# Kernel tuning notes

Measured on AMD Instinct MI355X. Metric: run time of the kernel, lower is better.

## Reference

```python
import jax, jax.numpy as jnp
import numpy as np

# config constants
S = 26            # output_size (fm_width == fm_height)
A = 5             # anchor_num
C = 80            # class_num
B = 64            # batch_size
T = 16            # GT boxes per image
DS = 32.0         # downsample_rate
IOU_THR = 0.5
SCALE_NOOBJ = 1.0
SCALE_OBJ = 5.0
ANCHOR_BOX = np.array([[1.32, 1.73], [3.19, 4.0], [5.05, 8.09], [9.47, 4.84], [11.2, 10.0]], dtype=np.float32)


def setup_inputs() -> dict:
    key = jax.random.key(0)
    ks = jax.random.split(key, 8)
    conf = jax.random.normal(ks[0], (B, S, S, A, 1), dtype=jnp.float32)
    pred_xy = jax.random.uniform(ks[1], (B, S, S, A, 2), dtype=jnp.float32) * S
    pred_wh = jax.random.uniform(ks[2], (B, S, S, A, 2), dtype=jnp.float32) * S + 0.5
    cls_score = jax.random.normal(ks[3], (B, S, S, A, C), dtype=jnp.float32)
    # GT boxes in PIXEL coords (module divides by downsample_rate): (x, y, w, h)
    xy = jax.random.uniform(ks[4], (B, T, 2), dtype=jnp.float32) * (S * DS)
    wh = jax.random.uniform(ks[5], (B, T, 2), dtype=jnp.float32) * (S * DS * 0.5) + DS
    true_object = jnp.concatenate([xy, wh], axis=-1)
    cls_idx = jax.random.randint(ks[6], (B, T), 0, C)
    true_label = jax.nn.one_hot(cls_idx, C, dtype=jnp.float32)
    # per-cell integer coords, row-major over the S*S grid
    p = jnp.arange(S * S)
    fm_cord = jnp.stack([p // S, p % S], axis=-1).astype(jnp.float32)  # [S*S, 2]
    anchors = jnp.asarray(ANCHOR_BOX)
    epoch = 1
    return {"epoch": epoch, "conf": conf, "pred_xy": pred_xy, "pred_wh": pred_wh,
            "cls_score": cls_score, "true_object": true_object, "true_label": true_label,
            "fm_cord": fm_cord, "anchors": anchors}


def _center_align_iou_wh(wh1, wh2):
    # IoU of two boxes whose centers are aligned: only (w, h) matter.
    inter = jnp.minimum(wh1[..., 0], wh2[..., 0]) * jnp.minimum(wh1[..., 1], wh2[..., 1])
    union = wh1[..., 0] * wh1[..., 1] + wh2[..., 0] * wh2[..., 1] - inter
    return inter / union


def _bce_with_logits(x, t):
    return jnp.maximum(x, 0.0) - x * t + jnp.log1p(jnp.exp(-jnp.abs(x)))


def _assign_targets(pred_wh, true_object, true_label, anchors):
    """Vectorized replacement of the per-box Python loops."""
    g = true_object / DS                                   # [B,T,4] in fm units
    gw, gh = g[..., 2], g[..., 3]
    i = jnp.clip(jnp.floor(g[..., 0]).astype(jnp.int32), 0, S - 1)  # int(x)
    j = jnp.clip(jnp.floor(g[..., 1]).astype(jnp.int32), 0, S - 1)  # int(y)
    b_idx = jnp.broadcast_to(jnp.arange(B)[:, None], (B, T))

    # anchor-vs-gt center-aligned IoU: [B,T,A]
    inter = jnp.minimum(gw[..., None], anchors[:, 0]) * jnp.minimum(gh[..., None], anchors[:, 1])
    union = (gw * gh)[..., None] + anchors[:, 0] * anchors[:, 1] - inter
    iou_a = inter / union
    best = jnp.argmax(iou_a, axis=-1)                      # [B,T]

    # predicted box at the BEST anchor cell (the original uses best_iou_index in
    # both the if- and else- branches), center-aligned IoU against the gt box
    pbest_wh = pred_wh[b_idx, i, j, best]                  # [B,T,2]
    iou_pg = _center_align_iou_wh(pbest_wh, g[..., 2:4])   # [B,T]

    aa = jnp.broadcast_to(jnp.arange(A), (B, T, A))
    is_best = aa == best[..., None]
    over = iou_a > IOU_THR
    scale_best = 2.0 - (gw / S) * (gh / S)                 # [B,T]

    mask_val = jnp.where(is_best, 1.0, jnp.where(over, -1.0, 0.0))
    scale_val = jnp.where(is_best, scale_best[..., None], jnp.where(over, -1.0, 0.0))

    bi = jnp.broadcast_to(b_idx[..., None], (B, T, A))
    ii = jnp.broadcast_to(i[..., None], (B, T, A))
    jj = jnp.broadcast_to(j[..., None], (B, T, A))

    obj_mask = jnp.zeros((B, S, S, A), jnp.float32).at[bi, ii, jj, aa].set(mask_val)
    scale_weight = jnp.zeros((B, S, S, A), jnp.float32).at[bi, ii, jj, aa].set(scale_val)

    # pred_gt_iou is written for the best anchor and for non-best anchors BELOW
    # the threshold (else-branch); over-threshold non-best anchors are skipped.
    write_iou = is_best | (~over)
    a_safe = jnp.where(write_iou, aa, A)  # out-of-bounds -> dropped
    pred_gt_iou = jnp.zeros((B, S, S, A), jnp.float32).at[bi, ii, jj, a_safe].set(
        jnp.broadcast_to(iou_pg[..., None], (B, T, A)), mode="drop")

    true_bbox = jnp.zeros((B, S, S, A, 4), jnp.float32).at[b_idx, i, j, best].set(g)
    true_score = jnp.zeros((B, S, S, A, C), jnp.float32).at[..., -1].set(1.0)
    true_score = true_score.at[b_idx, i, j, best].set(true_label)
    return obj_mask, scale_weight, pred_gt_iou, true_bbox, true_score


def _yolo_loss(epoch, conf, pred_xy, pred_wh, cls_score, true_object, true_label, fm_cord, anchors):
    obj_mask, scale_weight, pred_gt_iou, true_bbox, true_score = _assign_targets(
        pred_wh, true_object, true_label, anchors)

    N = S * S * A
    conf_f = conf.reshape(B, N, 1)
    pxy = pred_xy.reshape(B, N, 2)
    pwh = pred_wh.reshape(B, N, 2)
    tb = true_bbox.reshape(B, N, 4)
    m = obj_mask.reshape(B, N, 1)
    piou = pred_gt_iou.reshape(B, N, 1)
    sw = scale_weight.reshape(B, N, 1)
    ts = true_score.reshape(B, N, C).transpose(0, 2, 1)    # [B,C,N]
    cs = cls_score.reshape(B, N, C).transpose(0, 2, 1)     # [B,C,N]
    # mimics fm_cord.view(WH,2).repeat(1,A,1): whole grid tiled A times -> [N,2]
    fm = jnp.tile(fm_cord, (A, 1))

    noobj_loss = (SCALE_NOOBJ * (m == 0) * 0.5 * conf_f ** 2).sum() / B
    obj_loss = (SCALE_OBJ * (m == 1) * 0.5 * (conf_f - piou) ** 2).sum() / B
    gt_mask = (sw > 0).astype(conf.dtype)
    true_loss_xy = (SCALE_OBJ * 0.5 * gt_mask * sw *
                    _bce_with_logits(pxy - fm[None], tb[..., :2] - fm[None])).sum() / B
    true_loss_wh = (SCALE_OBJ * 0.5 * gt_mask * sw * (pwh - tb[..., 2:]) ** 2).sum() / B
    cls_gt_mask = gt_mask.transpose(0, 2, 1)               # [B,1,N]
    score_loss = (SCALE_OBJ * 0.5 * cls_gt_mask * (cs - ts) ** 2).sum() / B
    # NOTE: original code computes the averaged total then OVERWRITES it:
    total_loss = score_loss
    return (total_loss, noobj_loss / 4.0, obj_loss / 4.0, score_loss / 4.0,
            true_loss_xy / 4.0, true_loss_wh / 4.0)


def reference(epoch, conf, pred_xy, pred_wh, cls_score, true_object, true_label, fm_cord, anchors):
    return _yolo_loss(epoch, conf, pred_xy, pred_wh, cls_score, true_object, true_label, fm_cord, anchors)
```

## Files before the change

### kernel.cpp

```cpp
#include <hip/hip_runtime.h>
#include <math.h>

#define S 26
#define A 5
#define C 80
#define B 64
#define T 16
#define DSR 32.0f
#define N_CELLS (S * S)
#define N_PRED (S * S * A)
#define CONF_N (B * N_PRED)
#define CONF_N4 (CONF_N / 4)
#define NBT (B * T)
#define NBLK 256
#define BS 256
#define NWAVE (BS / 64)

__global__ __launch_bounds__(BS) void main_kernel(
        const float* __restrict__ conf,
        const float* __restrict__ pred_xy,
        const float* __restrict__ pred_wh,
        const float* __restrict__ cls_score,
        const float* __restrict__ true_object,
        const float* __restrict__ true_label,
        const float* __restrict__ anchors,
        float* __restrict__ partials) {
    const int tid = threadIdx.x;
    const int bid = blockIdx.x;
    const int gidx = bid * BS + tid;
    const int lane = tid & 63;
    const int wave = tid >> 6;

    float v0 = 0.f, v1 = 0.f, v2 = 0.f, v3 = 0.f, v4 = 0.f, v5 = 0.f;

    if (gidx < CONF_N4) {
        float4 c = ((const float4*)conf)[gidx];
        v0 = c.x * c.x + c.y * c.y + c.z * c.z + c.w * c.w;
    }

    if (gidx < NBT) {
        const int bt = gidx;
        const int b = bt >> 4;
        const int t = bt & 15;

        float4 to = ((const float4*)true_object)[bt];
        float gx = to.x / DSR, gy = to.y / DSR;
        float gw = to.z / DSR, gh = to.w / DSR;
        int i = min(max((int)floorf(gx), 0), S - 1);
        int j = min(max((int)floorf(gy), 0), S - 1);
        int ij = i * S + j;

        bool winner = true;
        #pragma unroll
        for (int t2 = 0; t2 < T; ++t2) {
            int ij2 = __shfl(ij, (lane & 48) + t2, 64);
            if (t2 > t && ij2 == ij) winner = false;
        }

        if (winner) {
            float iou_a[A];
            int best = 0;
            float bestv = -1.f;
            #pragma unroll
            for (int a = 0; a < A; ++a) {
                float aw = anchors[a * 2 + 0], ah = anchors[a * 2 + 1];
                float inter = fminf(gw, aw) * fminf(gh, ah);
                float uni = gw * gh + aw * ah - inter;
                float val = inter / uni;
                iou_a[a] = val;
                if (val > bestv) { bestv = val; best = a; }
            }

            size_t base = (size_t)b * N_PRED + (size_t)ij * A;

            #pragma unroll
            for (int a = 0; a < A; ++a) {
                if (a == best || iou_a[a] > 0.5f) {
                    float c = conf[base + a];
                    v1 += 0.5f * c * c;
                }
            }

            float2 pwh = ((const float2*)pred_wh)[base + best];
            float pw = pwh.x, ph = pwh.y;
            float inter = fminf(pw, gw) * fminf(ph, gh);
            float uni = pw * ph + gw * gh - inter;
            float iou_pg = inter / uni;
            float cbest = conf[base + best];
            float d = cbest - iou_pg;
            v2 = 0.5f * d * d;

            float sw = 2.0f - (gw / (float)S) * (gh / (float)S);
            if (sw > 0.f) {
                int n = ij * A + best;
                int p = n % N_CELLS;
                float fm0 = (float)(p / S);
                float fm1 = (float)(p % S);
                float2 pxy = ((const float2*)pred_xy)[base + best];
                float x0 = pxy.x - fm0, tt0 = gx - fm0;
                float x1 = pxy.y - fm1, tt1 = gy - fm1;
                float bce0 = fmaxf(x0, 0.f) - x0 * tt0 + log1pf(expf(-fabsf(x0)));
                float bce1 = fmaxf(x1, 0.f) - x1 * tt1 + log1pf(expf(-fabsf(x1)));
                v3 = sw * (bce0 + bce1);
                float dw = pw - gw, dh = ph - gh;
                v4 = sw * (dw * dw + dh * dh);

                const float4* cs4 = (const float4*)(cls_score + (base + best) * C);
                const float4* tl4 = (const float4*)(true_label + (size_t)bt * C);
                float sacc = 0.f;
                #pragma unroll
                for (int c4 = 0; c4 < C / 4; ++c4) {
                    float4 cc = cs4[c4];
                    float4 tl = tl4[c4];
                    float d0 = cc.x - tl.x, d1 = cc.y - tl.y;
                    float d2 = cc.z - tl.z, d3 = cc.w - tl.w;
                    sacc += d0 * d0 + d1 * d1 + d2 * d2 + d3 * d3;
                }
                v5 = sacc;
            }
        }
    }

    float vs[6] = {v0, v1, v2, v3, v4, v5};
    #pragma unroll
    for (int k = 0; k < 6; ++k) {
        float v = vs[k];
        #pragma unroll
        for (int off = 32; off >= 1; off >>= 1)
            v += __shfl_xor(v, off, 64);
        vs[k] = v;
    }
    __shared__ float sm[NWAVE * 6];
    if (lane == 0) {
        #pragma unroll
        for (int k = 0; k < 6; ++k) sm[wave * 6 + k] = vs[k];
    }
    __syncthreads();
    if (tid < 6) {
        float s = 0.f;
        #pragma unroll
        for (int w = 0; w < NWAVE; ++w) s += sm[w * 6 + tid];
        partials[tid * NBLK + bid] = s;
    }
}

__global__ __launch_bounds__(64) void finalize_kernel(
        const float* __restrict__ partials, float* __restrict__ out) {
    const int tid = threadIdx.x;
    float sums[6];
    #pragma unroll
    for (int k = 0; k < 6; ++k) {
        const float* p = partials + k * NBLK;
        float v = p[tid] + p[tid + 64] + p[tid + 128] + p[tid + 192];
        #pragma unroll
        for (int off = 32; off >= 1; off >>= 1)
            v += __shfl_xor(v, off, 64);
        sums[k] = v;
    }
    if (tid == 0) {
        const float invB = 1.0f / (float)B;
        float noobj = (0.5f * sums[0] - sums[1]) * invB;
        float obj   = 5.0f * sums[2] * invB;
        float xy    = 2.5f * sums[3] * invB;
        float wh    = 2.5f * sums[4] * invB;
        float score = 2.5f * sums[5] * invB;
        out[0] = score;
        out[1] = noobj * 0.25f;
        out[2] = obj * 0.25f;
        out[3] = score * 0.25f;
        out[4] = xy * 0.25f;
        out[5] = wh * 0.25f;
    }
}

extern "C" void kernel_launch(void* const* d_in, const int* in_sizes, int n_in,
                              void* d_out, int out_size, void* d_ws, size_t ws_size,
                              hipStream_t stream) {
    const float* conf        = (const float*)d_in[1];
    const float* pred_xy     = (const float*)d_in[2];
    const float* pred_wh     = (const float*)d_in[3];
    const float* cls_score   = (const float*)d_in[4];
    const float* true_object = (const float*)d_in[5];
    const float* true_label  = (const float*)d_in[6];
    const float* anchors     = (const float*)d_in[8];

    float* ws  = (float*)d_ws;
    float* out = (float*)d_out;

    hipLaunchKernelGGL(main_kernel, dim3(NBLK), dim3(BS), 0, stream,
                       conf, pred_xy, pred_wh, cls_score, true_object,
                       true_label, anchors, ws);
    hipLaunchKernelGGL(finalize_kernel, dim3(1), dim3(64), 0, stream, ws, out);
}
```

Measured before the change: 13.22 us.

## Fuse finalize into main kernel via flag-tagged partials polled by block zero

Merges the two-kernel reduction into one launch. Block 0 spins on per-block 64-bit packets tagged with a magic value and reduces them, then resets the flags for the next call. Worker blocks now split their work by range, so the GT-box threads are a separate slice after the conf slice and 216 worker blocks are used instead of 256. This removes the second launch and its gap, but depends on all 217 blocks being co-resident to avoid deadlock, and on the workspace not holding stale magic values.

New measurement: 14.05 us. 1.06x slower.

```diff
diff --git a/kernel.cpp b/kernel.cpp
--- a/kernel.cpp
+++ b/kernel.cpp
@@ -12,11 +12,13 @@
 #define CONF_N (B * N_PRED)
 #define CONF_N4 (CONF_N / 4)
 #define NBT (B * T)
-#define NBLK 256
 #define BS 256
-#define NWAVE (BS / 64)
-
-__global__ __launch_bounds__(BS) void main_kernel(
+#define NWORK 216
+#define NBLK (NWORK + 1)
+#define NFLAGS (NWORK * 6)
+#define MAGIC 0x9E3779B9u
+
+__global__ __launch_bounds__(BS) void yolo_fused(
         const float* __restrict__ conf,
         const float* __restrict__ pred_xy,
         const float* __restrict__ pred_wh,
@@ -24,104 +26,150 @@
         const float* __restrict__ true_object,
         const float* __restrict__ true_label,
         const float* __restrict__ anchors,
-        float* __restrict__ partials) {
+        unsigned long long* __restrict__ flags,
+        float* __restrict__ out) {
     const int tid = threadIdx.x;
     const int bid = blockIdx.x;
-    const int gidx = bid * BS + tid;
     const int lane = tid & 63;
     const int wave = tid >> 6;
-
-    float v0 = 0.f, v1 = 0.f, v2 = 0.f, v3 = 0.f, v4 = 0.f, v5 = 0.f;
-
-    if (gidx < CONF_N4) {
-        float4 c = ((const float4*)conf)[gidx];
-        v0 = c.x * c.x + c.y * c.y + c.z * c.z + c.w * c.w;
-    }
-
-    if (gidx < NBT) {
-        const int bt = gidx;
-        const int b = bt >> 4;
-        const int t = bt & 15;
-
-        float4 to = ((const float4*)true_object)[bt];
-        float gx = to.x / DSR, gy = to.y / DSR;
-        float gw = to.z / DSR, gh = to.w / DSR;
-        int i = min(max((int)floorf(gx), 0), S - 1);
-        int j = min(max((int)floorf(gy), 0), S - 1);
-        int ij = i * S + j;
-
-        bool winner = true;
-        #pragma unroll
-        for (int t2 = 0; t2 < T; ++t2) {
-            int ij2 = __shfl(ij, (lane & 48) + t2, 64);
-            if (t2 > t && ij2 == ij) winner = false;
-        }
-
-        if (winner) {
-            float iou_a[A];
-            int best = 0;
-            float bestv = -1.f;
+    __shared__ float sm[(BS / 64) * 6];
+
+    if (bid > 0) {
+        const int gidx = (bid - 1) * BS + tid;
+        float v0 = 0.f, v1 = 0.f, v2 = 0.f, v3 = 0.f, v4 = 0.f, v5 = 0.f;
+
+        if (gidx < CONF_N4) {
+            float4 c = ((const float4*)conf)[gidx];
+            v0 = c.x * c.x + c.y * c.y + c.z * c.z + c.w * c.w;
+        } else if (gidx < CONF_N4 + NBT) {
+            const int bt = gidx - CONF_N4;
+            const int b = bt >> 4;
+            const int t = bt & 15;
+
+            float4 to = ((const float4*)true_object)[bt];
+            float gx = to.x / DSR, gy = to.y / DSR;
+            float gw = to.z / DSR, gh = to.w / DSR;
+            int i = min(max((int)floorf(gx), 0), S - 1);
+            int j = min(max((int)floorf(gy), 0), S - 1);
+            int ij = i * S + j;
+
+            bool winner = true;
             #pragma unroll
-            for (int a = 0; a < A; ++a) {
-                float aw = anchors[a * 2 + 0], ah = anchors[a * 2 + 1];
-                float inter = fminf(gw, aw) * fminf(gh, ah);
-                float uni = gw * gh + aw * ah - inter;
-                float val = inter / uni;
-                iou_a[a] = val;
-                if (val > bestv) { bestv = val; best = a; }
+            for (int t2 = 0; t2 < T; ++t2) {
+                int ij2 = __shfl(ij, (lane & 48) + t2, 64);
+                if (t2 > t && ij2 == ij) winner = false;
             }
 
-            size_t base = (size_t)b * N_PRED + (size_t)ij * A;
-
-            #pragma unroll
-            for (int a = 0; a < A; ++a) {
-                if (a == best || iou_a[a] > 0.5f) {
-                    float c = conf[base + a];
-                    v1 += 0.5f * c * c;
+            if (winner) {
+                float iou_a[A];
+                int best = 0;
+                float bestv = -1.f;
+                #pragma unroll
+                for (int a = 0; a < A; ++a) {
+                    float aw = anchors[a * 2 + 0], ah = anchors[a * 2 + 1];
+                    float inter = fminf(gw, aw) * fminf(gh, ah);
+                    float uni = gw * gh + aw * ah - inter;
+                    float val = inter / uni;
+                    iou_a[a] = val;
+                    if (val > bestv) { bestv = val; best = a; }
+                }
+
+                size_t base = (size_t)b * N_PRED + (size_t)ij * A;
+
+                #pragma unroll
+                for (int a = 0; a < A; ++a) {
+                    if (a == best || iou_a[a] > 0.5f) {
+                        float c = conf[base + a];
+                        v1 += 0.5f * c * c;
+                    }
+                }
+
+                float2 pwh = ((const float2*)pred_wh)[base + best];
+                float pw = pwh.x, ph = pwh.y;
+                float inter = fminf(pw, gw) * fminf(ph, gh);
+                float uni = pw * ph + gw * gh - inter;
+                float iou_pg = inter / uni;
+                float cbest = conf[base + best];
+                float d = cbest - iou_pg;
+                v2 = 0.5f * d * d;
+
+                float sw = 2.0f - (gw / (float)S) * (gh / (float)S);
+                if (sw > 0.f) {
+                    int n = ij * A + best;
+                    int p = n % N_CELLS;
+                    float fm0 = (float)(p / S);
+                    float fm1 = (float)(p % S);
+                    float2 pxy = ((const float2*)pred_xy)[base + best];
+                    float x0 = pxy.x - fm0, tt0 = gx - fm0;
+                    float x1 = pxy.y - fm1, tt1 = gy - fm1;
+                    float bce0 = fmaxf(x0, 0.f) - x0 * tt0 + log1pf(expf(-fabsf(x0)));
+                    float bce1 = fmaxf(x1, 0.f) - x1 * tt1 + log1pf(expf(-fabsf(x1)));
+                    v3 = sw * (bce0 + bce1);
+                    float dw = pw - gw, dh = ph - gh;
+                    v4 = sw * (dw * dw + dh * dh);
+
+                    const float4* cs4 = (const float4*)(cls_score + (base + best) * C);
+                    const float4* tl4 = (const float4*)(true_label + (size_t)bt * C);
+                    float sacc = 0.f;
+                    #pragma unroll
+                    for (int c4 = 0; c4 < C / 4; ++c4) {
+                        float4 cc = cs4[c4];
+                        float4 tl = tl4[c4];
+                        float d0 = cc.x - tl.x, d1 = cc.y - tl.y;
+                        float d2 = cc.z - tl.z, d3 = cc.w - tl.w;
+                        sacc += d0 * d0 + d1 * d1 + d2 * d2 + d3 * d3;
+                    }
+                    v5 = sacc;
                 }
             }
-
-            float2 pwh = ((const float2*)pred_wh)[base + best];
-            float pw = pwh.x, ph = pwh.y;
-            float inter = fminf(pw, gw) * fminf(ph, gh);
-            float uni = pw * ph + gw * gh - inter;
-            float iou_pg = inter / uni;
-            float cbest = conf[base + best];
-            float d = cbest - iou_pg;
-            v2 = 0.5f * d * d;
-
-            float sw = 2.0f - (gw / (float)S) * (gh / (float)S);
-            if (sw > 0.f) {
-                int n = ij * A + best;
-                int p = n % N_CELLS;
-                float fm0 = (float)(p / S);
-                float fm1 = (float)(p % S);
-                float2 pxy = ((const float2*)pred_xy)[base + best];
-                float x0 = pxy.x - fm0, tt0 = gx - fm0;
-                float x1 = pxy.y - fm1, tt1 = gy - fm1;
-                float bce0 = fmaxf(x0, 0.f) - x0 * tt0 + log1pf(expf(-fabsf(x0)));
-                float bce1 = fmaxf(x1, 0.f) - x1 * tt1 + log1pf(expf(-fabsf(x1)));
-                v3 = sw * (bce0 + bce1);
-                float dw = pw - gw, dh = ph - gh;
-                v4 = sw * (dw * dw + dh * dh);
-
-                const float4* cs4 = (const float4*)(cls_score + (base + best) * C);
-                const float4* tl4 = (const float4*)(true_label + (size_t)bt * C);
-                float sacc = 0.f;
-                #pragma unroll
-                for (int c4 = 0; c4 < C / 4; ++c4) {
-                    float4 cc = cs4[c4];
-                    float4 tl = tl4[c4];
-                    float d0 = cc.x - tl.x, d1 = cc.y - tl.y;
-                    float d2 = cc.z - tl.z, d3 = cc.w - tl.w;
-                    sacc += d0 * d0 + d1 * d1 + d2 * d2 + d3 * d3;
-                }
-                v5 = sacc;
-            }
-        }
-    }
-
-    float vs[6] = {v0, v1, v2, v3, v4, v5};
+        }
+
+        float vs[6] = {v0, v1, v2, v3, v4, v5};
+        #pragma unroll
+        for (int k = 0; k < 6; ++k) {
+            float v = vs[k];
+            #pragma unroll
+            for (int off = 32; off >= 1; off >>= 1)
+                v += __shfl_xor(v, off, 64);
+            vs[k] = v;
+        }
+        if (lane == 0) {
+            #pragma unroll
+            for (int k = 0; k < 6; ++k) sm[wave * 6 + k] = vs[k];
+        }
+        __syncthreads();
+        if (tid < 6) {
+            float s = sm[0 * 6 + tid] + sm[1 * 6 + tid] +
+                      sm[2 * 6 + tid] + sm[3 * 6 + tid];
+            unsigned long long pkt =
+                ((unsigned long long)MAGIC << 32) |
+                (unsigned long long)__float_as_uint(s);
+            __hip_atomic_store(&flags[(bid - 1) * 6 + tid], pkt,
+                               __ATOMIC_RELEASE, __HIP_MEMORY_SCOPE_AGENT);
+        }
+        return;
+    }
+
+    float s0 = 0.f, s1 = 0.f, s2 = 0.f, s3 = 0.f, s4 = 0.f, s5 = 0.f;
+    for (int m = tid; m < NFLAGS; m += BS) {
+        unsigned long long v;
+        do {
+            v = __hip_atomic_load(&flags[m], __ATOMIC_ACQUIRE,
+                                  __HIP_MEMORY_SCOPE_AGENT);
+        } while ((unsigned)(v >> 32) != MAGIC);
+        __hip_atomic_store(&flags[m], 0ull, __ATOMIC_RELAXED,
+                           __HIP_MEMORY_SCOPE_AGENT);
+        float val = __uint_as_float((unsigned)(v & 0xFFFFFFFFull));
+        const int k = m % 6;
+        s0 += (k == 0) ? val : 0.f;
+        s1 += (k == 1) ? val : 0.f;
+        s2 += (k == 2) ? val : 0.f;
+        s3 += (k == 3) ? val : 0.f;
+        s4 += (k == 4) ? val : 0.f;
+        s5 += (k == 5) ? val : 0.f;
+    }
+
+    float vs[6] = {s0, s1, s2, s3, s4, s5};
     #pragma unroll
     for (int k = 0; k < 6; ++k) {
         float v = vs[k];
@@ -130,34 +178,16 @@
             v += __shfl_xor(v, off, 64);
         vs[k] = v;
     }
-    __shared__ float sm[NWAVE * 6];
     if (lane == 0) {
         #pragma unroll
         for (int k = 0; k < 6; ++k) sm[wave * 6 + k] = vs[k];
     }
     __syncthreads();
-    if (tid < 6) {
-        float s = 0.f;
-        #pragma unroll
-        for (int w = 0; w < NWAVE; ++w) s += sm[w * 6 + tid];
-        partials[tid * NBLK + bid] = s;
-    }
-}
-
-__global__ __launch_bounds__(64) void finalize_kernel(
-        const float* __restrict__ partials, float* __restrict__ out) {
-    const int tid = threadIdx.x;
-    float sums[6];
-    #pragma unroll
-    for (int k = 0; k < 6; ++k) {
-        const float* p = partials + k * NBLK;
-        float v = p[tid] + p[tid + 64] + p[tid + 128] + p[tid + 192];
-        #pragma unroll
-        for (int off = 32; off >= 1; off >>= 1)
-            v += __shfl_xor(v, off, 64);
-        sums[k] = v;
-    }
     if (tid == 0) {
+        float sums[6];
+        #pragma unroll
+        for (int k = 0; k < 6; ++k)
+            sums[k] = sm[0 * 6 + k] + sm[1 * 6 + k] + sm[2 * 6 + k] + sm[3 * 6 + k];
         const float invB = 1.0f / (float)B;
         float noobj = (0.5f * sums[0] - sums[1]) * invB;
         float obj   = 5.0f * sums[2] * invB;
@@ -184,11 +214,10 @@
     const float* true_label  = (const float*)d_in[6];
     const float* anchors     = (const float*)d_in[8];
 
-    float* ws  = (float*)d_ws;
+    unsigned long long* flags = (unsigned long long*)d_ws;
     float* out = (float*)d_out;
 
-    hipLaunchKernelGGL(main_kernel, dim3(NBLK), dim3(BS), 0, stream,
+    hipLaunchKernelGGL(yolo_fused, dim3(NBLK), dim3(BS), 0, stream,
                        conf, pred_xy, pred_wh, cls_score, true_object,
-                       true_label, anchors, ws);
-    hipLaunchKernelGGL(finalize_kernel, dim3(1), dim3(64), 0, stream, ws, out);
+                       true_label, anchors, flags, out);
 }
```
